# Kernel optimization log

Hardware: AMD Instinct MI355X
Metric: run time of the kernel (lower is better)

## Reference

```python
import jax, jax.numpy as jnp
import numpy as np

N = 50000          # nodes
E = 800000         # edges per metapath
M = 3              # metapaths
IN_DIM = 256
H = 8              # heads
D = 32             # out_dim per head
HID = 128          # semantic attention hidden
NEG_SLOPE = 0.2    # DGL GATConv default leaky_relu slope


def setup_inputs() -> dict:
    key = jax.random.key(0)
    ks = jax.random.split(key, 10)
    h = jax.random.normal(ks[0], (N, IN_DIM), dtype=jnp.float32)
    src = jax.random.randint(ks[1], (M, E), 0, N, dtype=jnp.int32)
    dst = jax.random.randint(ks[2], (M, E), 0, N, dtype=jnp.int32)
    s = 1.0 / np.sqrt(IN_DIM)
    fc_w = jax.random.normal(ks[3], (M, IN_DIM, H * D), dtype=jnp.float32) * s
    attn_l = jax.random.normal(ks[4], (M, H, D), dtype=jnp.float32) * 0.1
    attn_r = jax.random.normal(ks[5], (M, H, D), dtype=jnp.float32) * 0.1
    bias = jnp.zeros((M, H * D), dtype=jnp.float32)
    sem_w1 = jax.random.normal(ks[6], (H * D, HID), dtype=jnp.float32) * (1.0 / np.sqrt(H * D))
    sem_b1 = jnp.zeros((HID,), dtype=jnp.float32)
    sem_w2 = jax.random.normal(ks[7], (HID, 1), dtype=jnp.float32) * (1.0 / np.sqrt(HID))
    return {"h": h, "src": src, "dst": dst, "fc_w": fc_w, "attn_l": attn_l,
            "attn_r": attn_r, "bias": bias, "sem_w1": sem_w1, "sem_b1": sem_b1,
            "sem_w2": sem_w2}


def _gat(h, src, dst, fc_w, attn_l, attn_r, bias):
    # DGL GATConv (eval mode, dropout=0), activation=elu.
    feat = (h @ fc_w).reshape(N, H, D)                       # [N,H,D]
    el = jnp.sum(feat * attn_l, axis=-1)                     # [N,H]
    er = jnp.sum(feat * attn_r, axis=-1)                     # [N,H]
    e = jax.nn.leaky_relu(el[src] + er[dst], NEG_SLOPE)      # [E,H]
    # edge softmax over incoming edges of each dst node
    emax = jax.ops.segment_max(e, dst, num_segments=N)       # [N,H]
    emax = jnp.where(jnp.isfinite(emax), emax, 0.0)
    ee = jnp.exp(e - emax[dst])                              # [E,H]
    esum = jax.ops.segment_sum(ee, dst, num_segments=N)      # [N,H]
    alpha = ee / jnp.maximum(esum[dst], 1e-38)               # [E,H]
    msg = feat[src] * alpha[:, :, None]                      # [E,H,D]
    rst = jax.ops.segment_sum(msg, dst, num_segments=N)      # [N,H,D]
    rst = rst + bias.reshape(1, H, D)
    return jax.nn.elu(rst).reshape(N, H * D)                 # flatten heads


def reference(h, src, dst, fc_w, attn_l, attn_r, bias, sem_w1, sem_b1, sem_w2):
    gat_all = jax.vmap(_gat, in_axes=(None, 0, 0, 0, 0, 0, 0))
    z_m = gat_all(h, src, dst, fc_w, attn_l, attn_r, bias)   # [M,N,F]
    z_m = jnp.transpose(z_m, (1, 0, 2))                      # [N,M,F]
    # semantic attention
    w = jnp.tanh(z_m @ sem_w1 + sem_b1) @ sem_w2             # [N,M,1]
    w = w.mean(axis=0)                                       # [M,1]
    a_w = jax.nn.softmax(w, axis=0)                          # [M,1]
    z = jnp.sum(z_m * a_w[None, :, :], axis=1)               # [N,F]
    return z
```

## Files before the change

### kernel.cpp

```cpp
#include <hip/hip_runtime.h>
#include <math.h>

#define NN   50000
#define EE   800000
#define MM   3
#define KDIM 256
#define FF   256
#define HH   8
#define DD   32
#define HID  128
#define SLOPE 0.2f
#define BK   32
#define PAD  40
#define CAP  80

typedef unsigned short u16;
typedef unsigned int   u32;
typedef __attribute__((ext_vector_type(8))) short short8;
typedef __attribute__((ext_vector_type(4))) float floatx4;

__device__ __forceinline__ float eluf(float x) { return x > 0.f ? x : expm1f(x); }

__device__ __forceinline__ float b2f_lo(u32 u) {
    union { u32 i; float f; } v; v.i = u << 16; return v.f;
}
__device__ __forceinline__ float b2f_hi(u32 u) {
    union { u32 i; float f; } v; v.i = u & 0xffff0000u; return v.f;
}
__device__ __forceinline__ u16 f2b(float f) {
    union { float f; u32 i; } v; v.f = f;
    u32 lsb = (v.i >> 16) & 1u;
    v.i += 0x7fffu + lsb;
    return (u16)(v.i >> 16);
}
__device__ __forceinline__ u32 pack2(float lo, float hi) {
    return (u32)f2b(lo) | ((u32)f2b(hi) << 16);
}

__global__ __launch_bounds__(256) void k_cast_h(
    const float* __restrict__ hmat, u16* __restrict__ hb)
{
    long long i = ((long long)blockIdx.x * 256 + threadIdx.x) * 8;
    if (i >= (long long)NN * KDIM) return;
    float4 v0 = *(const float4*)(hmat + i);
    float4 v1 = *(const float4*)(hmat + i + 4);
    uint4 u;
    u.x = pack2(v0.x, v0.y); u.y = pack2(v0.z, v0.w);
    u.z = pack2(v1.x, v1.y); u.w = pack2(v1.z, v1.w);
    *(uint4*)(hb + i) = u;
}

__global__ __launch_bounds__(256) void k_cast_w(
    const float* __restrict__ fcw, u16* __restrict__ fcwt)
{
    int k = blockIdx.x, m = blockIdx.y, n = threadIdx.x;
    float v = fcw[((size_t)m * KDIM + k) * FF + n];
    fcwt[((size_t)m * FF + n) * KDIM + k] = f2b(v);
}

__global__ __launch_bounds__(128) void k_cast_w1(
    const float* __restrict__ w1, u16* __restrict__ w1t)
{
    int k = blockIdx.x, n = threadIdx.x;
    w1t[(size_t)n * KDIM + k] = f2b(w1[(size_t)k * HID + n]);
}

__global__ __launch_bounds__(256) void k_scatter_fixed(
    const int* __restrict__ src, const int* __restrict__ dst,
    int* __restrict__ cnt, u16* __restrict__ srt)
{
    long long eg = (long long)blockIdx.x * 256 + threadIdx.x;
    if (eg < (long long)MM * EE) {
        int m = (int)(eg / EE);
        int d = dst[eg];
        int slot = atomicAdd(&cnt[(size_t)m * NN + d], 1);
        if (slot < CAP) srt[(size_t)(m * CAP + slot) * NN + d] = (u16)src[eg];
    }
}

__global__ __launch_bounds__(256) void k_feat_all(
    const u16*   __restrict__ hb,
    const u16*   __restrict__ fcwt,
    const float* __restrict__ al,
    const float* __restrict__ ar,
    u16*   __restrict__ featb,
    float* __restrict__ el,
    float* __restrict__ er)
{
    __shared__ u16 As[128 * PAD];
    __shared__ u16 Bs[128 * PAD];

    const int n0 = blockIdx.x * 128;
    const int cy = blockIdx.y;
    const int m  = blockIdx.z;
    const int c_base = cy * 128;
    const int t = threadIdx.x;
    const int wave = t >> 6, lane = t & 63;
    const int wr = wave >> 1, wc = wave & 1;
    const int quad = lane >> 4, l15 = lane & 15;

    const u16* fcwt_m = fcwt + (size_t)m * FF * KDIM;
    const float* al_m = al + (size_t)m * HH * DD;
    const float* ar_m = ar + (size_t)m * HH * DD;

    floatx4 acc[4][4] = {};

    for (int k0 = 0; k0 < KDIM; k0 += BK) {
        __syncthreads();
        #pragma unroll
        for (int i = 0; i < 2; ++i) {
            int flat = i * 256 + t;
            int r = flat >> 2, seg = flat & 3;
            int n = n0 + r;
            uint4 u = make_uint4(0u, 0u, 0u, 0u);
            if (n < NN) u = *(const uint4*)(hb + (size_t)n * KDIM + k0 + seg * 8);
            *(uint4*)(&As[r * PAD + seg * 8]) = u;
        }
        #pragma unroll
        for (int i = 0; i < 2; ++i) {
            int flat = i * 256 + t;
            int r = flat >> 2, seg = flat & 3;
            uint4 u = *(const uint4*)(fcwt_m + (size_t)(c_base + r) * KDIM + k0 + seg * 8);
            *(uint4*)(&Bs[r * PAD + seg * 8]) = u;
        }
        __syncthreads();

        short8 afr[4], bfr[4];
        #pragma unroll
        for (int ti = 0; ti < 4; ++ti)
            afr[ti] = *(const short8*)(&As[(wr * 64 + ti * 16 + l15) * PAD + quad * 8]);
        #pragma unroll
        for (int tj = 0; tj < 4; ++tj)
            bfr[tj] = *(const short8*)(&Bs[(wc * 64 + tj * 16 + l15) * PAD + quad * 8]);
        #pragma unroll
        for (int ti = 0; ti < 4; ++ti)
            #pragma unroll
            for (int tj = 0; tj < 4; ++tj)
                acc[ti][tj] = __builtin_amdgcn_mfma_f32_16x16x32_bf16(
                    afr[ti], bfr[tj], acc[ti][tj], 0, 0, 0);
    }

    float alv[4], arv[4];
    #pragma unroll
    for (int tj = 0; tj < 4; ++tj) {
        int h = cy * 4 + wc * 2 + (tj >> 1);
        int dcol = (tj & 1) * 16 + l15;
        alv[tj] = al_m[h * DD + dcol];
        arv[tj] = ar_m[h * DD + dcol];
    }
    const int h0 = cy * 4 + wc * 2, h1 = h0 + 1;

    #pragma unroll
    for (int ti = 0; ti < 4; ++ti) {
        #pragma unroll
        for (int reg = 0; reg < 4; ++reg) {
            int n = n0 + wr * 64 + ti * 16 + quad * 4 + reg;
            bool ok = n < NN;
            if (ok) {
                #pragma unroll
                for (int tj = 0; tj < 4; ++tj) {
                    int c = c_base + wc * 64 + tj * 16 + l15;
                    featb[((size_t)m * NN + n) * FF + c] = f2b(acc[ti][tj][reg]);
                }
            }
            float pl0 = acc[ti][0][reg] * alv[0] + acc[ti][1][reg] * alv[1];
            float pl1 = acc[ti][2][reg] * alv[2] + acc[ti][3][reg] * alv[3];
            float pr0 = acc[ti][0][reg] * arv[0] + acc[ti][1][reg] * arv[1];
            float pr1 = acc[ti][2][reg] * arv[2] + acc[ti][3][reg] * arv[3];
            #pragma unroll
            for (int s = 1; s < 16; s <<= 1) {
                pl0 += __shfl_xor(pl0, s); pl1 += __shfl_xor(pl1, s);
                pr0 += __shfl_xor(pr0, s); pr1 += __shfl_xor(pr1, s);
            }
            if (l15 == 0 && ok) {
                el[((size_t)m * NN + n) * HH + h0] = pl0;
                el[((size_t)m * NN + n) * HH + h1] = pl1;
                er[((size_t)m * NN + n) * HH + h0] = pr0;
                er[((size_t)m * NN + n) * HH + h1] = pr1;
            }
        }
    }
}

__global__ __launch_bounds__(256) void k_aggr_all(
    const int* __restrict__ cnt,
    const u16* __restrict__ srt,
    const float* __restrict__ el,
    const float* __restrict__ er,
    const u16* __restrict__ featb,
    const float* __restrict__ bias,
    u16* __restrict__ z)
{
    __shared__ float alpha_s[4][2][CAP][HH];
    __shared__ int   srcoff[4][2][CAP];

    const int m = blockIdx.y;
    const int wave = threadIdx.x >> 6, lane = threadIdx.x & 63;
    const int half = lane >> 5, L = lane & 31;
    const int d = blockIdx.x * 8 + wave * 2 + half;

    const int deg = min(cnt[(size_t)m * NN + d], CAP);
    const float* el_m = el + (size_t)m * NN * HH;
    const u16* feat_m = featb + (size_t)m * NN * FF;

    #pragma unroll
    for (int i = 0; i < 3; ++i) {
        int slot = L + i * 32;
        if (slot < deg)
            srcoff[wave][half][slot] =
                (int)srt[(size_t)(m * CAP + slot) * NN + d] * FF;
    }

    const int hA = L & 7;
    const float er_d = er[((size_t)m * NN + d) * HH + hA];
    float esum_r = 0.f;
    const int nIter = (deg + 3) >> 2;
    for (int i = 0; i < nIter; ++i) {
        int j = i * 4 + (L >> 3);
        float e = 0.f;
        if (j < deg) {
            int so = srcoff[wave][half][j];
            float x = el_m[(size_t)(so >> 5) + hA] + er_d;
            x = x >= 0.f ? x : SLOPE * x;
            x = fminf(x, 60.f);
            e = expf(x);
            alpha_s[wave][half][j][hA] = e;
        }
        float g = e;
        g += __shfl_xor(g, 8); g += __shfl_xor(g, 16);
        esum_r += g;
    }
    float inv_r = 1.f / fmaxf(esum_r, 1e-38f);

    const float inv_g = __shfl(inv_r, (lane & 32) | (L >> 2));
    const int hB = L >> 2;
    float acc[8] = {0.f, 0.f, 0.f, 0.f, 0.f, 0.f, 0.f, 0.f};
    for (int j = 0; j < deg; ++j) {
        int so = srcoff[wave][half][j];
        float a = alpha_s[wave][half][j][hB];
        uint4 f = *(const uint4*)(feat_m + (size_t)so + L * 8);
        acc[0] += a * b2f_lo(f.x); acc[1] += a * b2f_hi(f.x);
        acc[2] += a * b2f_lo(f.y); acc[3] += a * b2f_hi(f.y);
        acc[4] += a * b2f_lo(f.z); acc[5] += a * b2f_hi(f.z);
        acc[6] += a * b2f_lo(f.w); acc[7] += a * b2f_hi(f.w);
    }
    #pragma unroll
    for (int k = 0; k < 8; ++k) acc[k] *= inv_g;

    const float4 b0 = *(const float4*)(bias + (size_t)m * FF + L * 8);
    const float4 b1 = *(const float4*)(bias + (size_t)m * FF + L * 8 + 4);
    uint4 o;
    o.x = pack2(eluf(acc[0] + b0.x), eluf(acc[1] + b0.y));
    o.y = pack2(eluf(acc[2] + b0.z), eluf(acc[3] + b0.w));
    o.z = pack2(eluf(acc[4] + b1.x), eluf(acc[5] + b1.y));
    o.w = pack2(eluf(acc[6] + b1.z), eluf(acc[7] + b1.w));
    *(uint4*)(z + ((size_t)m * NN + d) * FF + L * 8) = o;
}

__global__ __launch_bounds__(256) void k_sem_all(
    const u16* __restrict__ z,
    const u16* __restrict__ w1t,
    const float* __restrict__ b1,
    const float* __restrict__ w2,
    float* __restrict__ wsum)
{
    __shared__ u16 As[128 * PAD];
    __shared__ u16 Bs[128 * PAD];

    const int n0 = blockIdx.x * 128;
    const int m  = blockIdx.y;
    const int t = threadIdx.x;
    const int wave = t >> 6, lane = t & 63;
    const int wr = wave >> 1, wc = wave & 1;
    const int quad = lane >> 4, l15 = lane & 15;

    const u16* z_m = z + (size_t)m * NN * FF;

    floatx4 acc[4][4] = {};

    for (int k0 = 0; k0 < KDIM; k0 += BK) {
        __syncthreads();
        #pragma unroll
        for (int i = 0; i < 2; ++i) {
            int flat = i * 256 + t;
            int r = flat >> 2, seg = flat & 3;
            int n = n0 + r;
            uint4 u = make_uint4(0u, 0u, 0u, 0u);
            if (n < NN) u = *(const uint4*)(z_m + (size_t)n * FF + k0 + seg * 8);
            *(uint4*)(&As[r * PAD + seg * 8]) = u;
        }
        #pragma unroll
        for (int i = 0; i < 2; ++i) {
            int flat = i * 256 + t;
            int r = flat >> 2, seg = flat & 3;
            if (r < HID) {
                uint4 u = *(const uint4*)(w1t + (size_t)r * KDIM + k0 + seg * 8);
                *(uint4*)(&Bs[r * PAD + seg * 8]) = u;
            }
        }
        __syncthreads();

        short8 afr[4], bfr[4];
        #pragma unroll
        for (int ti = 0; ti < 4; ++ti)
            afr[ti] = *(const short8*)(&As[(wr * 64 + ti * 16 + l15) * PAD + quad * 8]);
        #pragma unroll
        for (int tj = 0; tj < 4; ++tj)
            bfr[tj] = *(const short8*)(&Bs[(wc * 64 + tj * 16 + l15) * PAD + quad * 8]);
        #pragma unroll
        for (int ti = 0; ti < 4; ++ti)
            #pragma unroll
            for (int tj = 0; tj < 4; ++tj)
                acc[ti][tj] = __builtin_amdgcn_mfma_f32_16x16x32_bf16(
                    afr[ti], bfr[tj], acc[ti][tj], 0, 0, 0);
    }

    float b1v[4], w2v[4];
    #pragma unroll
    for (int tj = 0; tj < 4; ++tj) {
        int c = wc * 64 + tj * 16 + l15;
        b1v[tj] = b1[c];
        w2v[tj] = w2[c];
    }
    float local = 0.f;
    #pragma unroll
    for (int ti = 0; ti < 4; ++ti) {
        #pragma unroll
        for (int reg = 0; reg < 4; ++reg) {
            int n = n0 + wr * 64 + ti * 16 + quad * 4 + reg;
            if (n < NN) {
                #pragma unroll
                for (int tj = 0; tj < 4; ++tj)
                    local += tanhf(acc[ti][tj][reg] + b1v[tj]) * w2v[tj];
            }
        }
    }
    #pragma unroll
    for (int s = 1; s < 64; s <<= 1) local += __shfl_xor(local, s);
    if (lane == 0) atomicAdd(&wsum[m], local);
}

__global__ __launch_bounds__(256) void k_combine(
    const u16* __restrict__ z, const float* __restrict__ wsum,
    float* __restrict__ out)
{
    float s0 = wsum[0] / (float)NN, s1 = wsum[1] / (float)NN, s2 = wsum[2] / (float)NN;
    float mx = fmaxf(s0, fmaxf(s1, s2));
    float e0 = expf(s0 - mx), e1 = expf(s1 - mx), e2 = expf(s2 - mx);
    float inv = 1.f / (e0 + e1 + e2);
    float aw[3] = { e0 * inv, e1 * inv, e2 * inv };

    long long idx = (long long)blockIdx.x * 256 + threadIdx.x;
    if (idx >= (long long)NN * 32) return;
    int n = (int)(idx >> 5), c = (int)(idx & 31) * 8;
    float acc[8] = {0.f, 0.f, 0.f, 0.f, 0.f, 0.f, 0.f, 0.f};
    #pragma unroll
    for (int m = 0; m < MM; ++m) {
        uint4 f = *(const uint4*)(z + ((size_t)m * NN + n) * FF + c);
        float a = aw[m];
        acc[0] += a * b2f_lo(f.x); acc[1] += a * b2f_hi(f.x);
        acc[2] += a * b2f_lo(f.y); acc[3] += a * b2f_hi(f.y);
        acc[4] += a * b2f_lo(f.z); acc[5] += a * b2f_hi(f.z);
        acc[6] += a * b2f_lo(f.w); acc[7] += a * b2f_hi(f.w);
    }
    float* op = out + (size_t)n * FF + c;
    *(float4*)op       = make_float4(acc[0], acc[1], acc[2], acc[3]);
    *(float4*)(op + 4) = make_float4(acc[4], acc[5], acc[6], acc[7]);
}

extern "C" void kernel_launch(void* const* d_in, const int* in_sizes, int n_in,
                              void* d_out, int out_size, void* d_ws, size_t ws_size,
                              hipStream_t stream)
{
    const float* hmat = (const float*)d_in[0];
    const int*   src  = (const int*)d_in[1];
    const int*   dst  = (const int*)d_in[2];
    const float* fcw  = (const float*)d_in[3];
    const float* al   = (const float*)d_in[4];
    const float* ar   = (const float*)d_in[5];
    const float* bias = (const float*)d_in[6];
    const float* w1   = (const float*)d_in[7];
    const float* b1   = (const float*)d_in[8];
    const float* w2   = (const float*)d_in[9];
    float* out = (float*)d_out;

    char* ws = (char*)d_ws;
    size_t off = 0;
    auto alloc = [&](size_t nbytes) {
        void* p = (void*)(ws + off);
        off = (off + nbytes + 255) & ~(size_t)255;
        return p;
    };
    float* el   = (float*)alloc((size_t)MM * NN * HH * 4);
    float* er   = (float*)alloc((size_t)MM * NN * HH * 4);
    float* wsum = (float*)alloc(256);
    int*   cnt  = (int*)alloc((size_t)MM * NN * 4);
    u16*   srt  = (u16*)alloc((size_t)MM * CAP * NN * 2);
    u16*   fcwt = (u16*)alloc((size_t)MM * KDIM * FF * 2);
    u16*   w1t  = (u16*)alloc((size_t)HID * KDIM * 2);
    u16*   hb   = (u16*)alloc((size_t)NN * KDIM * 2);
    u16*   featb= (u16*)alloc((size_t)MM * NN * FF * 2);
    u16*   z    = (u16*)alloc((size_t)MM * NN * FF * 2);

    hipMemsetAsync(wsum, 0, 256, stream);
    hipMemsetAsync(cnt, 0, (size_t)MM * NN * 4, stream);

    k_cast_h<<<(int)(((size_t)NN * KDIM / 8 + 255) / 256), 256, 0, stream>>>(hmat, hb);
    k_cast_w<<<dim3(KDIM, MM), 256, 0, stream>>>(fcw, fcwt);
    k_cast_w1<<<KDIM, 128, 0, stream>>>(w1, w1t);

    long long ne = (long long)MM * EE;
    k_scatter_fixed<<<(int)((ne + 255) / 256), 256, 0, stream>>>(src, dst, cnt, srt);

    k_feat_all<<<dim3((NN + 127) / 128, 2, MM), 256, 0, stream>>>(
        hb, fcwt, al, ar, featb, el, er);
    k_aggr_all<<<dim3(NN / 8, MM), 256, 0, stream>>>(cnt, srt, el, er, featb, bias, z);
    k_sem_all<<<dim3((NN + 127) / 128, MM), 256, 0, stream>>>(z, w1t, b1, w2, wsum);
    k_combine<<<(int)(((size_t)NN * 32 + 255) / 256), 256, 0, stream>>>(z, wsum, out);
}
```

Measured before the change: 601.2 us.

## Split GAT aggregation per head across blocks with edge-parallel lanes

The aggregation kernel is restructured so each block handles one attention head for 8 destination nodes, with a 32-lane group per node. Edges are spread across lanes: 4 edges in flight, 8 lanes covering the 32 features of the head, and the partial sums are combined with shuffles. The aim is more parallelism and memory-level concurrency per node, since the old loop walked edges serially with one wide load per lane. In exchange the grid is eight times larger, so source indices and edge offsets are re-read once per head. Each feature access is also a narrow 8-byte gather instead of a full 512-byte row.

```diff
diff --git a/kernel.cpp b/kernel.cpp
--- a/kernel.cpp
+++ b/kernel.cpp
@@ -191,70 +191,63 @@
     const float* __restrict__ bias,
     u16* __restrict__ z)
 {
-    __shared__ float alpha_s[4][2][CAP][HH];
-    __shared__ int   srcoff[4][2][CAP];
-
-    const int m = blockIdx.y;
-    const int wave = threadIdx.x >> 6, lane = threadIdx.x & 63;
-    const int half = lane >> 5, L = lane & 31;
-    const int d = blockIdx.x * 8 + wave * 2 + half;
+    __shared__ float alpha_s[8][CAP];
+    __shared__ int   eoff_s[8][CAP];
+
+    const int h = blockIdx.x;
+    const int m = blockIdx.z;
+    const int g = threadIdx.x >> 5;
+    const int L = threadIdx.x & 31;
+    const int d = blockIdx.y * 8 + g;
 
     const int deg = min(cnt[(size_t)m * NN + d], CAP);
     const float* el_m = el + (size_t)m * NN * HH;
     const u16* feat_m = featb + (size_t)m * NN * FF;
 
-    #pragma unroll
-    for (int i = 0; i < 3; ++i) {
-        int slot = L + i * 32;
-        if (slot < deg)
-            srcoff[wave][half][slot] =
-                (int)srt[(size_t)(m * CAP + slot) * NN + d] * FF;
-    }
-
-    const int hA = L & 7;
-    const float er_d = er[((size_t)m * NN + d) * HH + hA];
-    float esum_r = 0.f;
-    const int nIter = (deg + 3) >> 2;
-    for (int i = 0; i < nIter; ++i) {
-        int j = i * 4 + (L >> 3);
+    for (int i = L; i < deg; i += 32)
+        eoff_s[g][i] = (int)srt[(size_t)(m * CAP + i) * NN + d] * HH + h;
+
+    const float er_d = er[((size_t)m * NN + d) * HH + h];
+    float esum = 0.f;
+    for (int i = 0; i < deg; i += 32) {
+        int j = i + L;
         float e = 0.f;
         if (j < deg) {
-            int so = srcoff[wave][half][j];
-            float x = el_m[(size_t)(so >> 5) + hA] + er_d;
+            float x = el_m[eoff_s[g][j]] + er_d;
             x = x >= 0.f ? x : SLOPE * x;
             x = fminf(x, 60.f);
             e = expf(x);
-            alpha_s[wave][half][j][hA] = e;
-        }
-        float g = e;
-        g += __shfl_xor(g, 8); g += __shfl_xor(g, 16);
-        esum_r += g;
-    }
-    float inv_r = 1.f / fmaxf(esum_r, 1e-38f);
-
-    const float inv_g = __shfl(inv_r, (lane & 32) | (L >> 2));
-    const int hB = L >> 2;
-    float acc[8] = {0.f, 0.f, 0.f, 0.f, 0.f, 0.f, 0.f, 0.f};
-    for (int j = 0; j < deg; ++j) {
-        int so = srcoff[wave][half][j];
-        float a = alpha_s[wave][half][j][hB];
-        uint4 f = *(const uint4*)(feat_m + (size_t)so + L * 8);
-        acc[0] += a * b2f_lo(f.x); acc[1] += a * b2f_hi(f.x);
-        acc[2] += a * b2f_lo(f.y); acc[3] += a * b2f_hi(f.y);
-        acc[4] += a * b2f_lo(f.z); acc[5] += a * b2f_hi(f.z);
-        acc[6] += a * b2f_lo(f.w); acc[7] += a * b2f_hi(f.w);
-    }
-    #pragma unroll
-    for (int k = 0; k < 8; ++k) acc[k] *= inv_g;
-
-    const float4 b0 = *(const float4*)(bias + (size_t)m * FF + L * 8);
-    const float4 b1 = *(const float4*)(bias + (size_t)m * FF + L * 8 + 4);
-    uint4 o;
-    o.x = pack2(eluf(acc[0] + b0.x), eluf(acc[1] + b0.y));
-    o.y = pack2(eluf(acc[2] + b0.z), eluf(acc[3] + b0.w));
-    o.z = pack2(eluf(acc[4] + b1.x), eluf(acc[5] + b1.y));
-    o.w = pack2(eluf(acc[6] + b1.z), eluf(acc[7] + b1.w));
-    *(uint4*)(z + ((size_t)m * NN + d) * FF + L * 8) = o;
+            alpha_s[g][j] = e;
+        }
+        float t_ = e;
+        t_ += __shfl_xor(t_, 1);  t_ += __shfl_xor(t_, 2);
+        t_ += __shfl_xor(t_, 4);  t_ += __shfl_xor(t_, 8);
+        t_ += __shfl_xor(t_, 16);
+        esum += t_;
+    }
+    const float inv = 1.f / fmaxf(esum, 1e-38f);
+
+    const int e4 = L >> 3, c4 = L & 7;
+    float a0 = 0.f, a1 = 0.f, a2 = 0.f, a3 = 0.f;
+    for (int j = e4; j < deg; j += 4) {
+        float a = alpha_s[g][j];
+        uint2 f = *(const uint2*)(feat_m + (size_t)eoff_s[g][j] * 32 + c4 * 4);
+        a0 += a * b2f_lo(f.x); a1 += a * b2f_hi(f.x);
+        a2 += a * b2f_lo(f.y); a3 += a * b2f_hi(f.y);
+    }
+    a0 += __shfl_xor(a0, 8); a0 += __shfl_xor(a0, 16);
+    a1 += __shfl_xor(a1, 8); a1 += __shfl_xor(a1, 16);
+    a2 += __shfl_xor(a2, 8); a2 += __shfl_xor(a2, 16);
+    a3 += __shfl_xor(a3, 8); a3 += __shfl_xor(a3, 16);
+
+    if (e4 == 0) {
+        const int c = h * 32 + c4 * 4;
+        float4 b = *(const float4*)(bias + (size_t)m * FF + c);
+        uint2 o;
+        o.x = pack2(eluf(a0 * inv + b.x), eluf(a1 * inv + b.y));
+        o.y = pack2(eluf(a2 * inv + b.z), eluf(a3 * inv + b.w));
+        *(uint2*)(z + ((size_t)m * NN + d) * FF + c) = o;
+    }
 }
 
 __global__ __launch_bounds__(256) void k_sem_all(
@@ -414,7 +407,7 @@
 
     k_feat_all<<<dim3((NN + 127) / 128, 2, MM), 256, 0, stream>>>(
         hb, fcwt, al, ar, featb, el, er);
-    k_aggr_all<<<dim3(NN / 8, MM), 256, 0, stream>>>(cnt, srt, el, er, featb, bias, z);
+    k_aggr_all<<<dim3(HH, NN / 8, MM), 256, 0, stream>>>(cnt, srt, el, er, featb, bias, z);
     k_sem_all<<<dim3((NN + 127) / 128, MM), 256, 0, stream>>>(z, w1t, b1, w2, wsum);
     k_combine<<<(int)(((size_t)NN * 32 + 255) / 256), 256, 0, stream>>>(z, wsum, out);
 }
```

New measurement: 797.6 us. +32.7%, slower.
